# Performance work log

Hardware: AMD Instinct MI355X
Metric: run time of the kernel (lower is better)

The kernel has to match this reference:

```python
import jax, jax.numpy as jnp
import numpy as np

B, T, D = 32, 1024, 512  # batch, max_X (sequence), encoder width (== rnn width)
H = 10                   # hidden units of first attention Dense


def setup_inputs() -> dict:
    key = jax.random.key(0)
    k1, k2, k3, k4 = jax.random.split(key, 4)
    return {
        "cbhg_encoding": jax.random.normal(k1, (B, T, D), dtype=jnp.float32),
        "attention_rnn_output": jax.random.normal(k2, (B, D), dtype=jnp.float32),
        "W1": jax.random.normal(k3, (2 * D, H), dtype=jnp.float32) * (1.0 / np.sqrt(2 * D)),
        "b1": jnp.zeros((H,), dtype=jnp.float32),
        "W2": jax.random.normal(k4, (H, 1), dtype=jnp.float32) * (1.0 / np.sqrt(H)),
        "b2": jnp.zeros((1,), dtype=jnp.float32),
    }


def reference(cbhg_encoding, attention_rnn_output, W1, b1, W2, b2):
    b, t, d = cbhg_encoding.shape
    # RepeatVector(max_X): [B, D] -> [B, T, D]
    rnn_rep = jnp.broadcast_to(attention_rnn_output[:, None, :], (b, t, d))
    # Concatenate(axis=-1): [B, T, 2D]
    attn_in = jnp.concatenate([cbhg_encoding, rnn_rep], axis=-1)
    # Dense(10, tanh) -> Dense(1, relu): energies [B, T, 1]
    e = jnp.tanh(jnp.einsum("btf,fh->bth", attn_in, W1) + b1)
    energies = jax.nn.relu(jnp.einsum("bth,ho->bto", e, W2) + b2)
    # softmax over the sequence axis (attention weights over T)
    attention_weights = jax.nn.softmax(energies, axis=1)  # [B, T, 1]
    # Dot(axes=1): contract sequence axis -> context [B, 1, D]
    context = jnp.einsum("bti,btd->bid", attention_weights, cbhg_encoding)
    # Reshape rnn output to match context shape [B, 1, D]
    rnn_reshaped = attention_rnn_output.reshape(b, 1, d)
    return (context, rnn_reshaped)
```

## Files before the change

kernel.cpp:

```cpp
#include <hip/hip_runtime.h>

#define BB 32
#define TT 1024
#define DD 512
#define HH 10
#define WP 12
#define CHUNK 64
#define NCH (TT / CHUNK)


__global__ __launch_bounds__(256) void k0_init(
    const float* __restrict__ rnn, const float* __restrict__ W1,
    const float* __restrict__ b1, float* __restrict__ out,
    float* __restrict__ cbh, float* __restrict__ wpad) {
  const int b = blockIdx.x;
  const int tid = threadIdx.x;

  const float r0 = rnn[b * DD + tid];
  const float r1 = rnn[b * DD + tid + 256];

  out[BB * DD + b * DD + tid] = r0;
  out[BB * DD + b * DD + tid + 256] = r1;

  if (tid < 16 * WP) {
    const int idx = b * 16 * WP + tid;
    const int f = idx / WP;
    const int h = idx % WP;
    wpad[idx] = (h < HH) ? W1[f * HH + h] : 0.f;
  }

  float s[HH];
#pragma unroll
  for (int h = 0; h < HH; ++h)
    s[h] = r0 * W1[(DD + tid) * HH + h] + r1 * W1[(DD + tid + 256) * HH + h];

  __shared__ float red[256][HH];
#pragma unroll
  for (int h = 0; h < HH; ++h) red[tid][h] = s[h];
  __syncthreads();
  for (int off = 128; off > 0; off >>= 1) {
    if (tid < off) {
#pragma unroll
      for (int h = 0; h < HH; ++h) red[tid][h] += red[tid + off][h];
    }
    __syncthreads();
  }
  if (tid < HH) cbh[b * HH + tid] = red[0][tid] + b1[tid];
}

__global__ __launch_bounds__(256, 2) void k1_fused(
    const float* __restrict__ x, const float* __restrict__ wpad,
    const float* __restrict__ cbh, const float* __restrict__ W2,
    const float* __restrict__ b2, float* __restrict__ pc,
    float* __restrict__ sc) {
  const int b = blockIdx.x >> 4;
  const int tc = blockIdx.x & 15;
  const int lane = threadIdx.x & 63;
  const int wv = __builtin_amdgcn_readfirstlane(threadIdx.x >> 6);

  __shared__ float hpart[4][CHUNK][13];
  __shared__ float wgt[CHUNK];

  const int row = b * TT + tc * CHUNK + lane;
  const float* xr = x + (size_t)row * DD + wv * 128;
  const float* wp = wpad + wv * 128 * WP;

  float acc[HH];
#pragma unroll
  for (int h = 0; h < HH; ++h) acc[h] = 0.f;

#pragma unroll 4
  for (int k = 0; k < 32; ++k) {
    const float4 xv = *reinterpret_cast<const float4*>(xr + k * 4);
    const float xa[4] = {xv.x, xv.y, xv.z, xv.w};
#pragma unroll
    for (int j = 0; j < 4; ++j) {
      const float4 wa = *reinterpret_cast<const float4*>(wp + (k * 4 + j) * WP);
      const float4 wb = *reinterpret_cast<const float4*>(wp + (k * 4 + j) * WP + 4);
      const float2 wc = *reinterpret_cast<const float2*>(wp + (k * 4 + j) * WP + 8);
      const float xs = xa[j];
      acc[0] = fmaf(xs, wa.x, acc[0]);
      acc[1] = fmaf(xs, wa.y, acc[1]);
      acc[2] = fmaf(xs, wa.z, acc[2]);
      acc[3] = fmaf(xs, wa.w, acc[3]);
      acc[4] = fmaf(xs, wb.x, acc[4]);
      acc[5] = fmaf(xs, wb.y, acc[5]);
      acc[6] = fmaf(xs, wb.z, acc[6]);
      acc[7] = fmaf(xs, wb.w, acc[7]);
      acc[8] = fmaf(xs, wc.x, acc[8]);
      acc[9] = fmaf(xs, wc.y, acc[9]);
    }
  }

#pragma unroll
  for (int h = 0; h < HH; ++h) hpart[wv][lane][h] = acc[h];
  __syncthreads();

  if (threadIdx.x < 64) {
    float e = b2[0];
#pragma unroll
    for (int h = 0; h < HH; ++h) {
      const float v = hpart[0][lane][h] + hpart[1][lane][h] +
                      hpart[2][lane][h] + hpart[3][lane][h] + cbh[b * HH + h];
      const float z = __expf(2.f * v);
      const float th = 1.f - 2.f / (z + 1.f);
      e = fmaf(th, W2[h], e);
    }
    float w = __expf(fmaxf(e, 0.f));
    wgt[lane] = w;
#pragma unroll
    for (int off = 32; off > 0; off >>= 1) w += __shfl_xor(w, off, 64);
    if (lane == 0) sc[b * NCH + tc] = w;
  }
  __syncthreads();

  const int d0 = threadIdx.x * 2;
  const float* xb = x + (size_t)(b * TT + tc * CHUNK) * DD + d0;
  float ax = 0.f, ay = 0.f;
#pragma unroll 8
  for (int r = 0; r < CHUNK; ++r) {
    const float wr = wgt[r];
    const float2 xv = *reinterpret_cast<const float2*>(xb + (size_t)r * DD);
    ax = fmaf(wr, xv.x, ax);
    ay = fmaf(wr, xv.y, ay);
  }
  *reinterpret_cast<float2*>(pc + (size_t)(b * NCH + tc) * DD + d0) =
      make_float2(ax, ay);
}

__global__ __launch_bounds__(256) void k2_combine(
    const float* __restrict__ pc, const float* __restrict__ sc,
    float* __restrict__ out) {
  const int b = blockIdx.x;
  const int d0 = threadIdx.x * 2;

  float ssum = 0.f;
#pragma unroll
  for (int c = 0; c < NCH; ++c) ssum += sc[b * NCH + c];

  float ax = 0.f, ay = 0.f;
#pragma unroll
  for (int c = 0; c < NCH; ++c) {
    const float2 v =
        *reinterpret_cast<const float2*>(pc + (size_t)(b * NCH + c) * DD + d0);
    ax += v.x;
    ay += v.y;
  }
  const float inv = 1.f / ssum;
  *reinterpret_cast<float2*>(out + b * DD + d0) = make_float2(ax * inv, ay * inv);
}

extern "C" void kernel_launch(void* const* d_in, const int* in_sizes, int n_in,
                              void* d_out, int out_size, void* d_ws,
                              size_t ws_size, hipStream_t stream) {
  const float* cbhg = (const float*)d_in[0];
  const float* rnn = (const float*)d_in[1];
  const float* W1 = (const float*)d_in[2];
  const float* b1 = (const float*)d_in[3];
  const float* W2 = (const float*)d_in[4];
  const float* b2 = (const float*)d_in[5];
  float* out = (float*)d_out;

  float* wpad = (float*)d_ws;
  float* cbh = wpad + DD * WP;
  float* pc = wpad + 6656;
  float* sc = pc + BB * NCH * DD;

  k0_init<<<BB, 256, 0, stream>>>(rnn, W1, b1, out, cbh, wpad);
  k1_fused<<<BB * NCH, 256, 0, stream>>>(cbhg, wpad, cbh, W2, b2, pc, sc);
  k2_combine<<<BB, 256, 0, stream>>>(pc, sc, out);
}
```

Measured before the change: 117.9 us.

## Fuse init, main and combine kernels into one cooperative launch with grid sync

Merges the three launches into a single cooperative kernel. Each block now recomputes the rnn projection bias and stages the padded W1 into shared memory itself, and a grid-wide sync replaces the separate combine kernel. This is meant to remove launch overhead and the global wpad/cbh round trip. In exchange every block does redundant W1 staging and reduction work, and the cooperative launch needs all 512 blocks to be co-resident; if that launch fails, the code falls back to two kernels.

```diff
diff --git a/kernel.cpp b/kernel.cpp
--- a/kernel.cpp
+++ b/kernel.cpp
@@ -1,69 +1,74 @@
 #include <hip/hip_runtime.h>
+#include <hip/hip_cooperative_groups.h>
+
+namespace cg = cooperative_groups;
 
 #define BB 32
 #define TT 1024
 #define DD 512
 #define HH 10
-#define WP 12
+#define WPAD 12
 #define CHUNK 64
 #define NCH (TT / CHUNK)
 
 
-__global__ __launch_bounds__(256) void k0_init(
-    const float* __restrict__ rnn, const float* __restrict__ W1,
-    const float* __restrict__ b1, float* __restrict__ out,
-    float* __restrict__ cbh, float* __restrict__ wpad) {
-  const int b = blockIdx.x;
+template <bool COOP>
+__global__ __launch_bounds__(256, 2) void attn_k(
+    const float* __restrict__ x, const float* __restrict__ rnn,
+    const float* __restrict__ W1, const float* __restrict__ b1,
+    const float* __restrict__ W2, const float* __restrict__ b2,
+    float* __restrict__ pc, float* __restrict__ sc, float* __restrict__ out) {
+  const int b = blockIdx.x >> 4;
+  const int tc = blockIdx.x & (NCH - 1);
   const int tid = threadIdx.x;
+  const int lane = tid & 63;
+  const int wv = tid >> 6;
+
+  __shared__ float wlds[DD * WPAD];
+  __shared__ float upool[4 * CHUNK * 13];
+  __shared__ float cbh_s[HH];
+  __shared__ float wgt[CHUNK];
 
   const float r0 = rnn[b * DD + tid];
   const float r1 = rnn[b * DD + tid + 256];
-
-  out[BB * DD + b * DD + tid] = r0;
-  out[BB * DD + b * DD + tid + 256] = r1;
-
-  if (tid < 16 * WP) {
-    const int idx = b * 16 * WP + tid;
-    const int f = idx / WP;
-    const int h = idx % WP;
-    wpad[idx] = (h < HH) ? W1[f * HH + h] : 0.f;
-  }
-
-  float s[HH];
-#pragma unroll
-  for (int h = 0; h < HH; ++h)
-    s[h] = r0 * W1[(DD + tid) * HH + h] + r1 * W1[(DD + tid + 256) * HH + h];
-
-  __shared__ float red[256][HH];
-#pragma unroll
-  for (int h = 0; h < HH; ++h) red[tid][h] = s[h];
-  __syncthreads();
-  for (int off = 128; off > 0; off >>= 1) {
-    if (tid < off) {
-#pragma unroll
-      for (int h = 0; h < HH; ++h) red[tid][h] += red[tid + off][h];
-    }
+  if (tc == 0) {
+    out[BB * DD + b * DD + tid] = r0;
+    out[BB * DD + b * DD + tid + 256] = r1;
+  }
+
+#pragma unroll
+  for (int i = 0; i < DD * HH / 256; ++i) {
+    const int idx = i * 256 + tid;
+    const int f = idx / HH;
+    const int h = idx - f * HH;
+    wlds[f * WPAD + h] = W1[idx];
+  }
+
+  {
+    float s[HH];
+#pragma unroll
+    for (int h = 0; h < HH; ++h)
+      s[h] = r0 * W1[(DD + tid) * HH + h] + r1 * W1[(DD + tid + 256) * HH + h];
+    float* red = upool;
+#pragma unroll
+    for (int h = 0; h < HH; ++h) red[tid * HH + h] = s[h];
     __syncthreads();
-  }
-  if (tid < HH) cbh[b * HH + tid] = red[0][tid] + b1[tid];
-}
-
-__global__ __launch_bounds__(256, 2) void k1_fused(
-    const float* __restrict__ x, const float* __restrict__ wpad,
-    const float* __restrict__ cbh, const float* __restrict__ W2,
-    const float* __restrict__ b2, float* __restrict__ pc,
-    float* __restrict__ sc) {
-  const int b = blockIdx.x >> 4;
-  const int tc = blockIdx.x & 15;
-  const int lane = threadIdx.x & 63;
-  const int wv = __builtin_amdgcn_readfirstlane(threadIdx.x >> 6);
-
-  __shared__ float hpart[4][CHUNK][13];
-  __shared__ float wgt[CHUNK];
-
+    for (int off = 128; off > 0; off >>= 1) {
+      if (tid < off) {
+#pragma unroll
+        for (int h = 0; h < HH; ++h)
+          red[tid * HH + h] += red[(tid + off) * HH + h];
+      }
+      __syncthreads();
+    }
+    if (tid < HH) cbh_s[tid] = red[tid] + b1[tid];
+    __syncthreads();
+  }
+
+  float (*hp)[CHUNK][13] = (float (*)[CHUNK][13])upool;
   const int row = b * TT + tc * CHUNK + lane;
   const float* xr = x + (size_t)row * DD + wv * 128;
-  const float* wp = wpad + wv * 128 * WP;
+  const float* wp = wlds + wv * 128 * WPAD;
 
   float acc[HH];
 #pragma unroll
@@ -75,9 +80,12 @@
     const float xa[4] = {xv.x, xv.y, xv.z, xv.w};
 #pragma unroll
     for (int j = 0; j < 4; ++j) {
-      const float4 wa = *reinterpret_cast<const float4*>(wp + (k * 4 + j) * WP);
-      const float4 wb = *reinterpret_cast<const float4*>(wp + (k * 4 + j) * WP + 4);
-      const float2 wc = *reinterpret_cast<const float2*>(wp + (k * 4 + j) * WP + 8);
+      const float4 wa =
+          *reinterpret_cast<const float4*>(wp + (k * 4 + j) * WPAD);
+      const float4 wb =
+          *reinterpret_cast<const float4*>(wp + (k * 4 + j) * WPAD + 4);
+      const float2 wc =
+          *reinterpret_cast<const float2*>(wp + (k * 4 + j) * WPAD + 8);
       const float xs = xa[j];
       acc[0] = fmaf(xs, wa.x, acc[0]);
       acc[1] = fmaf(xs, wa.y, acc[1]);
@@ -93,15 +101,15 @@
   }
 
 #pragma unroll
-  for (int h = 0; h < HH; ++h) hpart[wv][lane][h] = acc[h];
+  for (int h = 0; h < HH; ++h) hp[wv][lane][h] = acc[h];
   __syncthreads();
 
-  if (threadIdx.x < 64) {
+  if (tid < 64) {
     float e = b2[0];
 #pragma unroll
     for (int h = 0; h < HH; ++h) {
-      const float v = hpart[0][lane][h] + hpart[1][lane][h] +
-                      hpart[2][lane][h] + hpart[3][lane][h] + cbh[b * HH + h];
+      const float v = hp[0][lane][h] + hp[1][lane][h] + hp[2][lane][h] +
+                      hp[3][lane][h] + cbh_s[h];
       const float z = __expf(2.f * v);
       const float th = 1.f - 2.f / (z + 1.f);
       e = fmaf(th, W2[h], e);
@@ -114,7 +122,7 @@
   }
   __syncthreads();
 
-  const int d0 = threadIdx.x * 2;
+  const int d0 = tid * 2;
   const float* xb = x + (size_t)(b * TT + tc * CHUNK) * DD + d0;
   float ax = 0.f, ay = 0.f;
 #pragma unroll 8
@@ -126,6 +134,27 @@
   }
   *reinterpret_cast<float2*>(pc + (size_t)(b * NCH + tc) * DD + d0) =
       make_float2(ax, ay);
+
+  if constexpr (COOP) {
+    __threadfence();
+    cg::this_grid().sync();
+    if (tc == 0) {
+      float ssum = 0.f;
+#pragma unroll
+      for (int c = 0; c < NCH; ++c) ssum += sc[b * NCH + c];
+      float cx = 0.f, cy = 0.f;
+#pragma unroll
+      for (int c = 0; c < NCH; ++c) {
+        const float2 v = *reinterpret_cast<const float2*>(
+            pc + (size_t)(b * NCH + c) * DD + d0);
+        cx += v.x;
+        cy += v.y;
+      }
+      const float inv = 1.f / ssum;
+      *reinterpret_cast<float2*>(out + b * DD + d0) =
+          make_float2(cx * inv, cy * inv);
+    }
+  }
 }
 
 __global__ __launch_bounds__(256) void k2_combine(
@@ -133,11 +162,9 @@
     float* __restrict__ out) {
   const int b = blockIdx.x;
   const int d0 = threadIdx.x * 2;
-
   float ssum = 0.f;
 #pragma unroll
   for (int c = 0; c < NCH; ++c) ssum += sc[b * NCH + c];
-
   float ax = 0.f, ay = 0.f;
 #pragma unroll
   for (int c = 0; c < NCH; ++c) {
@@ -147,7 +174,8 @@
     ay += v.y;
   }
   const float inv = 1.f / ssum;
-  *reinterpret_cast<float2*>(out + b * DD + d0) = make_float2(ax * inv, ay * inv);
+  *reinterpret_cast<float2*>(out + b * DD + d0) =
+      make_float2(ax * inv, ay * inv);
 }
 
 extern "C" void kernel_launch(void* const* d_in, const int* in_sizes, int n_in,
@@ -161,12 +189,17 @@
   const float* b2 = (const float*)d_in[5];
   float* out = (float*)d_out;
 
-  float* wpad = (float*)d_ws;
-  float* cbh = wpad + DD * WP;
-  float* pc = wpad + 6656;
+  float* pc = (float*)d_ws;
   float* sc = pc + BB * NCH * DD;
 
-  k0_init<<<BB, 256, 0, stream>>>(rnn, W1, b1, out, cbh, wpad);
-  k1_fused<<<BB * NCH, 256, 0, stream>>>(cbhg, wpad, cbh, W2, b2, pc, sc);
-  k2_combine<<<BB, 256, 0, stream>>>(pc, sc, out);
+  void* args[] = {(void*)&cbhg, (void*)&rnn, (void*)&W1, (void*)&b1,
+                  (void*)&W2,   (void*)&b2,  (void*)&pc, (void*)&sc,
+                  (void*)&out};
+  hipError_t err = hipLaunchCooperativeKernel(
+      (const void*)attn_k<true>, dim3(BB * NCH), dim3(256), args, 0, stream);
+  if (err != hipSuccess) {
+    attn_k<false><<<BB * NCH, 256, 0, stream>>>(cbhg, rnn, W1, b1, W2, b2, pc,
+                                                sc, out);
+    k2_combine<<<BB, 256, 0, stream>>>(pc, sc, out);
+  }
 }
```

Measured after the change: 230.9 us. +95.9%, slower.
